# Performance work log

Hardware: AMD Instinct MI355X
Metric: run time of the kernel (lower is better)

## Reference

```python
import jax, jax.numpy as jnp
import numpy as np

N = 100000   # nodes
E = 600000   # edges (before self loops)
D = 128      # dim_latent = H*F
H = 4        # heads
F = 32       # out_feats per head
L = 3        # num GATConv layers (conv_0 + 2)


def setup_inputs() -> dict:
    key = jax.random.key(0)
    ks = jax.random.split(key, 10)
    return {
        "weights": jax.random.normal(ks[0], (N,), jnp.float32),
        "lin_W": jax.random.normal(ks[1], (D, 1), jnp.float32) * 0.1,
        "lin_b": jnp.zeros((D,), jnp.float32),
        "fc_W": jax.random.normal(ks[2], (L, D, D), jnp.float32) * (1.0 / np.sqrt(D)),
        "attn_l": jax.random.normal(ks[3], (L, H, F), jnp.float32) * 0.1,
        "attn_r": jax.random.normal(ks[4], (L, H, F), jnp.float32) * 0.1,
        "conv_b": jnp.zeros((L, D), jnp.float32),
        "pred_W": jax.random.normal(ks[5], (1, D), jnp.float32) * 0.1,
        "pred_b": jnp.zeros((1,), jnp.float32),
        "src": jax.random.randint(ks[6], (E,), 0, N, jnp.int32),
        "dst": jax.random.randint(ks[7], (E,), 0, N, jnp.int32),
    }


def _leaky(x, slope):
    return jnp.where(x >= 0, x, slope * x)


def _gat_conv(x, fc_W, attn_l, attn_r, bias, src, dst):
    # DGL GATConv: bias-free fc, per-head additive attention, edge softmax over dst
    h = (x @ fc_W.T).reshape(N, H, F)                      # [N,H,F]
    el = jnp.sum(h * attn_l[None], axis=-1)                # [N,H]
    er = jnp.sum(h * attn_r[None], axis=-1)                # [N,H]
    e = _leaky(el[src] + er[dst], 0.2)                     # [Etot,H]
    m = jax.ops.segment_max(e, dst, num_segments=N)        # [N,H]
    a = jnp.exp(e - m[dst])                                # [Etot,H]
    s = jax.ops.segment_sum(a, dst, num_segments=N)        # [N,H]
    alpha = a / s[dst]                                     # [Etot,H]
    msg = h[src] * alpha[:, :, None]                       # [Etot,H,F]
    out = jax.ops.segment_sum(msg, dst, num_segments=N)    # [N,H,F]
    out = out + bias.reshape(H, F)[None]
    return out.reshape(N, H * F)


def reference(weights, lin_W, lin_b, fc_W, attn_l, attn_r, conv_b, pred_W, pred_b, src, dst):
    # add self loops (dgl.add_self_loop)
    loop = jnp.arange(N, dtype=src.dtype)
    s_full = jnp.concatenate([src, loop])
    d_full = jnp.concatenate([dst, loop])

    x = weights[:, None] @ lin_W.T + lin_b                 # [N,D]
    for i in range(L):
        if i > 0:
            x = _leaky(x, 0.01)                            # nn.LeakyReLU default
        x = _gat_conv(x, fc_W[i], attn_l[i], attn_r[i], conv_b[i], s_full, d_full)
    logits = x @ pred_W.T + pred_b                         # [N,1]
    return logits
```

## Files before the change

### kernel.cpp

```cpp
#include <hip/hip_runtime.h>
#include <hip/hip_bf16.h>
#include <math.h>


__device__ __forceinline__ float leaky02(float x) {
    return x >= 0.f ? x : 0.2f * x;
}
__device__ __forceinline__ float leaky01(float x) {
    return x >= 0.f ? x : 0.01f * x;
}

__device__ __forceinline__ unsigned short f2bf(float f) {
    unsigned u = __float_as_uint(f);
    unsigned r = u + 0x7FFFu + ((u >> 16) & 1u);
    return (unsigned short)(r >> 16);
}
__device__ __forceinline__ float bf2f(unsigned short s) {
    return __uint_as_float(((unsigned)s) << 16);
}

typedef __attribute__((ext_vector_type(8))) short bf16x8;
typedef __attribute__((ext_vector_type(8))) unsigned short u16x8;
typedef __attribute__((ext_vector_type(4))) float f32x4;

__global__ __launch_bounds__(256) void init_split_kernel(
    int* __restrict__ deg, int N, const float* __restrict__ W,
    short* __restrict__ Wh, short* __restrict__ Wl, int n)
{
    int i = blockIdx.x * 256 + threadIdx.x;
    if (i < N) deg[i] = 1;
    if (i < n) {
        int l    = i >> 14;
        int p    = i & 16383;
        int j    = p & 7;
        int lane = (p >> 3) & 63;
        int c    = (p >> 9) & 7;
        int kk   = p >> 12;
        int mr   = lane & 15;
        int quad = lane >> 4;
        int row  = c * 16 + mr;
        int d    = kk * 32 + quad * 8 + j;
        float f = W[(size_t)l * 16384 + row * 128 + d];
        unsigned short hi = f2bf(f);
        Wh[i] = (short)hi;
        Wl[i] = (short)f2bf(f - bf2f(hi));
    }
}

__global__ __launch_bounds__(1024) void mlr_prep_kernel(
    const float* __restrict__ fc_W, const float* __restrict__ attn_l,
    const float* __restrict__ attn_r, short* __restrict__ Mh,
    short* __restrict__ Ml)
{
    int l = blockIdx.x;
    const float* W  = fc_W + (size_t)(l + 1) * 16384;
    const float* al = attn_l + (l + 1) * 128;
    const float* ar = attn_r + (l + 1) * 128;
    short* mh = Mh + (size_t)l * 16 * 128;
    short* ml = Ml + (size_t)l * 16 * 128;
    int t = threadIdx.x;
    int r = t >> 7;
    int d = t & 127;
    int hh = r & 3;
    const float* av = (r < 4) ? al : ar;
    float s = 0.f;
#pragma unroll
    for (int f = 0; f < 32; ++f)
        s += W[(size_t)(hh * 32 + f) * 128 + d] * av[hh * 32 + f];
    unsigned short hi = f2bf(s);
    mh[r * 128 + d] = (short)hi;
    ml[r * 128 + d] = (short)f2bf(s - bf2f(hi));
    mh[(r + 8) * 128 + d] = 0;
    ml[(r + 8) * 128 + d] = 0;
}

__global__ __launch_bounds__(256) void deg_count_slot_kernel(
    const int* __restrict__ dst, int* __restrict__ deg,
    int* __restrict__ slot, int E)
{
    int i = blockIdx.x * 256 + threadIdx.x;
    if (i < E) slot[i] = atomicAdd(&deg[dst[i]], 1);
}

#define SCAN_TILE 1024

__global__ __launch_bounds__(256) void scanA_kernel(
    const int* __restrict__ deg, int* __restrict__ bsum, int N)
{
    __shared__ int ws[4];
    int b = blockIdx.x, t = threadIdx.x;
    int base = b * SCAN_TILE + t * 4;
    int s = 0;
#pragma unroll
    for (int k = 0; k < 4; ++k) {
        int i = base + k;
        if (i < N) s += deg[i];
    }
#pragma unroll
    for (int m = 32; m >= 1; m >>= 1) s += __shfl_xor(s, m, 64);
    if ((t & 63) == 0) ws[t >> 6] = s;
    __syncthreads();
    if (t == 0) bsum[b] = ws[0] + ws[1] + ws[2] + ws[3];
}

__global__ __launch_bounds__(1024) void scanB_kernel(
    int* __restrict__ bsum, int* __restrict__ bpre, int* __restrict__ rowp,
    int NB, int N)
{
    __shared__ int sh[1024];
    int t = threadIdx.x;
    int v = (t < NB) ? bsum[t] : 0;
    sh[t] = v;
    __syncthreads();
    for (int off = 1; off < 1024; off <<= 1) {
        int u = (t >= off) ? sh[t - off] : 0;
        __syncthreads();
        sh[t] += u;
        __syncthreads();
    }
    if (t < NB) bpre[t] = sh[t] - v;
    if (t == 1023) rowp[N] = sh[1023];
}

__global__ __launch_bounds__(256) void scanC_kernel(
    const int* __restrict__ deg, const int* __restrict__ bpre,
    int* __restrict__ rowp, int* __restrict__ col, int N)
{
    __shared__ int sh[256];
    int b = blockIdx.x, t = threadIdx.x;
    int base = b * SCAN_TILE + t * 4;
    int v[4];
#pragma unroll
    for (int k = 0; k < 4; ++k) {
        int i = base + k;
        v[k] = (i < N) ? deg[i] : 0;
    }
    int tsum = v[0] + v[1] + v[2] + v[3];
    sh[t] = tsum;
    __syncthreads();
    for (int off = 1; off < 256; off <<= 1) {
        int u = (t >= off) ? sh[t - off] : 0;
        __syncthreads();
        sh[t] += u;
        __syncthreads();
    }
    int pre = bpre[b] + sh[t] - tsum;
#pragma unroll
    for (int k = 0; k < 4; ++k) {
        int i = base + k;
        if (i < N) {
            rowp[i] = pre;
            col[pre] = i;
        }
        pre += v[k];
    }
}

__global__ __launch_bounds__(256) void scatter2_kernel(
    const int* __restrict__ src, const int* __restrict__ dst,
    const int* __restrict__ slot, const int* __restrict__ rowp,
    int* __restrict__ col, int E)
{
    int i = blockIdx.x * 256 + threadIdx.x;
    if (i < E) col[rowp[dst[i]] + slot[i]] = src[i];
}

__global__ __launch_bounds__(1024) void rank1_prep_kernel(
    const float* __restrict__ lW, const float* __restrict__ lb,
    const float* __restrict__ W0, const float* __restrict__ al,
    const float* __restrict__ ar, const float* __restrict__ cb2,
    const float* __restrict__ pW, const float* __restrict__ pb,
    float* __restrict__ c1, float* __restrict__ c2, float* __restrict__ prm)
{
    __shared__ float sh1[128], sh2[128], sh3[128], sh4[128], sh5[128];
    int t = threadIdx.x;
    int j = t >> 3, sub = t & 7;
    float s1 = 0.f, s2 = 0.f;
    int d0 = sub * 16;
#pragma unroll
    for (int k = 0; k < 16; ++k) {
        float wv = W0[j * 128 + d0 + k];
        s1 += lW[d0 + k] * wv;
        s2 += lb[d0 + k] * wv;
    }
#pragma unroll
    for (int m = 1; m <= 4; m <<= 1) {
        s1 += __shfl_xor(s1, m, 64);
        s2 += __shfl_xor(s2, m, 64);
    }
    if (sub == 0) {
        c1[j] = s1; c2[j] = s2;
        sh1[j] = s1 * al[j]; sh2[j] = s2 * al[j];
        sh3[j] = s1 * ar[j]; sh4[j] = s2 * ar[j];
        sh5[j] = cb2[j] * pW[j];
    }
    __syncthreads();
    if (t < 4) {
        float p = 0.f, q = 0.f, r = 0.f, s = 0.f;
        for (int f = 0; f < 32; ++f) {
            p += sh1[t * 32 + f]; q += sh2[t * 32 + f];
            r += sh3[t * 32 + f]; s += sh4[t * 32 + f];
        }
        prm[t] = p; prm[4 + t] = q; prm[8 + t] = r; prm[12 + t] = s;
    }
    if (t == 0) {
        float cs = 0.f;
        for (int k = 0; k < 128; ++k) cs += sh5[k];
        prm[16] = cs + pb[0];
    }
}

__global__ __launch_bounds__(256) void agg0_kernel(
    const float* __restrict__ w, const float* __restrict__ c1,
    const float* __restrict__ c2, const float* __restrict__ prm,
    const int* __restrict__ rowp, const int* __restrict__ col,
    const float* __restrict__ bias, unsigned short* __restrict__ xout, int N)
{
    const int lane = threadIdx.x & 63;
    const int q    = lane >> 4;
    const int l16  = lane & 15;
    const int v    = blockIdx.x * 16 + (threadIdx.x >> 6) * 4 + q;
    if (v >= N) return;

    const int r0 = rowp[v], r1 = rowp[v + 1];
    const int head = l16 >> 2;
    const int f0   = l16 * 8;
    const float pl = prm[head],     ql = prm[4 + head];
    const float pr = prm[8 + head], qr = prm[12 + head];

    const float wv  = w[v];
    const float erq = wv * pr + qr;
    const float mref = leaky02(wv * pl + ql + erq);

    float S = 0.f, Sw = 0.f;
    float w_cur = wv;
    for (int j = r0; j < r1; ++j) {
        int jn = (j + 1 < r1) ? (j + 1) : j;
        float w_nxt = w[col[jn]];

        float e = leaky02(w_cur * pl + ql + erq);
        float d = fminf(e - mref, 80.f);
        float p = __expf(d);
        S += p; Sw += p * w_cur;
        w_cur = w_nxt;
    }
    const float t = Sw / S;

    float4 a0 = *reinterpret_cast<const float4*>(&c1[f0]);
    float4 a1 = *reinterpret_cast<const float4*>(&c1[f0 + 4]);
    float4 g0 = *reinterpret_cast<const float4*>(&c2[f0]);
    float4 g1 = *reinterpret_cast<const float4*>(&c2[f0 + 4]);
    float4 b0 = *reinterpret_cast<const float4*>(&bias[f0]);
    float4 b1 = *reinterpret_cast<const float4*>(&bias[f0 + 4]);
    const float aa[8] = {a0.x, a0.y, a0.z, a0.w, a1.x, a1.y, a1.z, a1.w};
    const float gg[8] = {g0.x, g0.y, g0.z, g0.w, g1.x, g1.y, g1.z, g1.w};
    const float bb[8] = {b0.x, b0.y, b0.z, b0.w, b1.x, b1.y, b1.z, b1.w};

    u16x8 o;
#pragma unroll
    for (int k = 0; k < 8; ++k)
        o[k] = f2bf(leaky01(t * aa[k] + gg[k] + bb[k]));
    *reinterpret_cast<u16x8*>(&xout[(size_t)v * 128 + f0]) = o;
}

__global__ __launch_bounds__(256) void gemm_mfma_kernel(
    const unsigned short* __restrict__ xb, const short* __restrict__ Wh,
    const short* __restrict__ Wl, const short* __restrict__ Mh,
    const short* __restrict__ Ml, unsigned short* __restrict__ hb,
    float* __restrict__ el, float* __restrict__ er,
    const float* __restrict__ pW, float* __restrict__ yel,
    int N, int mode)
{
    const int lane = threadIdx.x & 63;
    const int wv   = threadIdx.x >> 6;
    const int m0   = blockIdx.x * 128 + wv * 32;
    const int mr   = lane & 15;
    const int quad = lane >> 4;

    int r0 = m0 + mr;      if (r0 > N - 1) r0 = N - 1;
    int r1 = m0 + 16 + mr; if (r1 > N - 1) r1 = N - 1;
    const unsigned short* xp0 = xb + (size_t)r0 * 128 + quad * 8;
    const unsigned short* xp1 = xb + (size_t)r1 * 128 + quad * 8;

    f32x4 acc0[8], acc1[8], acce0, acce1;
#pragma unroll
    for (int c = 0; c < 8; ++c) {
        acc0[c] = (f32x4){0.f, 0.f, 0.f, 0.f};
        acc1[c] = (f32x4){0.f, 0.f, 0.f, 0.f};
    }
    acce0 = (f32x4){0.f, 0.f, 0.f, 0.f};
    acce1 = (f32x4){0.f, 0.f, 0.f, 0.f};

#pragma unroll
    for (int kk = 0; kk < 4; ++kk) {
        bf16x8 a0 = *reinterpret_cast<const bf16x8*>(xp0 + kk * 32);
        bf16x8 a1 = *reinterpret_cast<const bf16x8*>(xp1 + kk * 32);

        const int kb = kk * 32 + quad * 8;
        bf16x8 bh[8], bl[8];
#pragma unroll
        for (int c = 0; c < 8; ++c) {
            const size_t wo = (size_t)((kk * 8 + c) * 64 + lane) * 8;
            bh[c] = *reinterpret_cast<const bf16x8*>(Wh + wo);
            bl[c] = *reinterpret_cast<const bf16x8*>(Wl + wo);
        }
        bf16x8 eh = *reinterpret_cast<const bf16x8*>(Mh + (size_t)mr * 128 + kb);
        bf16x8 eo = *reinterpret_cast<const bf16x8*>(Ml + (size_t)mr * 128 + kb);
#pragma unroll
        for (int c = 0; c < 8; ++c) {
            acc0[c] = __builtin_amdgcn_mfma_f32_16x16x32_bf16(a0, bh[c], acc0[c], 0, 0, 0);
            acc0[c] = __builtin_amdgcn_mfma_f32_16x16x32_bf16(a0, bl[c], acc0[c], 0, 0, 0);
            acc1[c] = __builtin_amdgcn_mfma_f32_16x16x32_bf16(a1, bh[c], acc1[c], 0, 0, 0);
            acc1[c] = __builtin_amdgcn_mfma_f32_16x16x32_bf16(a1, bl[c], acc1[c], 0, 0, 0);
        }
        acce0 = __builtin_amdgcn_mfma_f32_16x16x32_bf16(a0, eh, acce0, 0, 0, 0);
        acce0 = __builtin_amdgcn_mfma_f32_16x16x32_bf16(a0, eo, acce0, 0, 0, 0);
        acce1 = __builtin_amdgcn_mfma_f32_16x16x32_bf16(a1, eh, acce1, 0, 0, 0);
        acce1 = __builtin_amdgcn_mfma_f32_16x16x32_bf16(a1, eo, acce1, 0, 0, 0);
    }

    if (mode == 0) {
#pragma unroll
        for (int i = 0; i < 4; ++i) {
            int rowA = m0 + quad * 4 + i;
            if (rowA < N) {
                unsigned short* hp = hb + (size_t)rowA * 128 + mr;
#pragma unroll
                for (int c = 0; c < 8; ++c) hp[c * 16] = f2bf(acc0[c][i]);
                if (mr < 4)       el[(size_t)rowA * 4 + mr]       = acce0[i];
                else if (mr < 8)  er[(size_t)rowA * 4 + (mr - 4)] = acce0[i];
            }
            int rowB = m0 + 16 + quad * 4 + i;
            if (rowB < N) {
                unsigned short* hp = hb + (size_t)rowB * 128 + mr;
#pragma unroll
                for (int c = 0; c < 8; ++c) hp[c * 16] = f2bf(acc1[c][i]);
                if (mr < 4)       el[(size_t)rowB * 4 + mr]       = acce1[i];
                else if (mr < 8)  er[(size_t)rowB * 4 + (mr - 4)] = acce1[i];
            }
        }
    } else {
        float pw[8];
#pragma unroll
        for (int c = 0; c < 8; ++c) pw[c] = pW[mr + c * 16];
#pragma unroll
        for (int i = 0; i < 4; ++i) {
            int rowA = m0 + quad * 4 + i;
            {
                float y[4];
#pragma unroll
                for (int h = 0; h < 4; ++h)
                    y[h] = acc0[2 * h][i] * pw[2 * h] + acc0[2 * h + 1][i] * pw[2 * h + 1];
#pragma unroll
                for (int d = 1; d < 16; d <<= 1) {
#pragma unroll
                    for (int h = 0; h < 4; ++h) y[h] += __shfl_xor(y[h], d, 64);
                }
                if (rowA < N) {
                    if (mr < 4) {
                        float2 o; o.x = y[mr]; o.y = acce0[i];
                        *reinterpret_cast<float2*>(&yel[(size_t)rowA * 8 + mr * 2]) = o;
                    } else if (mr < 8) {
                        er[(size_t)rowA * 4 + (mr - 4)] = acce0[i];
                    }
                }
            }
            int rowB = m0 + 16 + quad * 4 + i;
            {
                float y[4];
#pragma unroll
                for (int h = 0; h < 4; ++h)
                    y[h] = acc1[2 * h][i] * pw[2 * h] + acc1[2 * h + 1][i] * pw[2 * h + 1];
#pragma unroll
                for (int d = 1; d < 16; d <<= 1) {
#pragma unroll
                    for (int h = 0; h < 4; ++h) y[h] += __shfl_xor(y[h], d, 64);
                }
                if (rowB < N) {
                    if (mr < 4) {
                        float2 o; o.x = y[mr]; o.y = acce1[i];
                        *reinterpret_cast<float2*>(&yel[(size_t)rowB * 8 + mr * 2]) = o;
                    } else if (mr < 8) {
                        er[(size_t)rowB * 4 + (mr - 4)] = acce1[i];
                    }
                }
            }
        }
    }
}

__global__ __launch_bounds__(256) void agg_mid_kernel(
    const unsigned short* __restrict__ hb, const float* __restrict__ el,
    const float* __restrict__ er, const int* __restrict__ rowp,
    const int* __restrict__ col, const float* __restrict__ bias,
    unsigned short* __restrict__ xout, int N)
{
    const int lane = threadIdx.x & 63;
    const int q    = lane >> 4;
    const int l16  = lane & 15;
    const int v    = blockIdx.x * 16 + (threadIdx.x >> 6) * 4 + q;
    if (v >= N) return;

    const int r0 = rowp[v], r1 = rowp[v + 1];
    const int head = l16 >> 2;
    const int f0   = l16 * 8;
    const float erq = er[(size_t)v * 4 + head];
    const float el_self = el[(size_t)v * 4 + head];
    const float mref = leaky02(el_self + erq);

    float s = 0.f;
    float acc[8];
#pragma unroll
    for (int k = 0; k < 8; ++k) acc[k] = 0.f;

    float elA = el_self;
    u16x8 hvA = *reinterpret_cast<const u16x8*>(&hb[(size_t)v * 128 + f0]);
    int jB = (r0 + 1 < r1) ? r0 + 1 : r1 - 1;
    int uB = col[jB];
    float elB = el[(size_t)uB * 4 + head];
    u16x8 hvB = *reinterpret_cast<const u16x8*>(&hb[(size_t)uB * 128 + f0]);

    for (int j = r0; j < r1; j += 2) {
        int jA2 = (j + 2 < r1) ? j + 2 : r1 - 1;
        int uA2 = col[jA2];
        float elA2 = el[(size_t)uA2 * 4 + head];
        u16x8 hvA2 = *reinterpret_cast<const u16x8*>(&hb[(size_t)uA2 * 128 + f0]);

        {
            float e = leaky02(elA + erq);
            float d = fminf(e - mref, 80.f);
            float p = __expf(d);
            s += p;
#pragma unroll
            for (int k = 0; k < 8; ++k) acc[k] += p * bf2f(hvA[k]);
        }

        if (j + 1 < r1) {
            int jB2 = (j + 3 < r1) ? j + 3 : r1 - 1;
            int uB2 = col[jB2];
            float elB2 = el[(size_t)uB2 * 4 + head];
            u16x8 hvB2 = *reinterpret_cast<const u16x8*>(&hb[(size_t)uB2 * 128 + f0]);

            float e = leaky02(elB + erq);
            float d = fminf(e - mref, 80.f);
            float p = __expf(d);
            s += p;
#pragma unroll
            for (int k = 0; k < 8; ++k) acc[k] += p * bf2f(hvB[k]);

            elB = elB2; hvB = hvB2;
        }
        elA = elA2; hvA = hvA2;
    }
    const float is = 1.f / s;

    float4 b0 = *reinterpret_cast<const float4*>(&bias[f0]);
    float4 b1 = *reinterpret_cast<const float4*>(&bias[f0 + 4]);
    const float bb[8] = {b0.x, b0.y, b0.z, b0.w, b1.x, b1.y, b1.z, b1.w};

    u16x8 o;
#pragma unroll
    for (int k = 0; k < 8; ++k) o[k] = f2bf(leaky01(acc[k] * is + bb[k]));
    *reinterpret_cast<u16x8*>(&xout[(size_t)v * 128 + f0]) = o;
}

__global__ __launch_bounds__(256) void agg2_kernel(
    const float* __restrict__ yel, const float* __restrict__ er,
    const int* __restrict__ rowp, const int* __restrict__ col,
    const float* __restrict__ prm, float* __restrict__ logits, int N)
{
    const int lane = threadIdx.x & 63;
    const int q    = lane >> 4;
    const int l16  = lane & 15;
    const int v    = blockIdx.x * 16 + (threadIdx.x >> 6) * 4 + q;
    if (v >= N) return;

    const int r0 = rowp[v], r1 = rowp[v + 1];
    const int head = l16 >> 2;
    const float erq = er[(size_t)v * 4 + head];

    float2 curA = *reinterpret_cast<const float2*>(&yel[(size_t)v * 8 + head * 2]);
    const float mref = leaky02(curA.y + erq);

    int jB = (r0 + 1 < r1) ? r0 + 1 : r1 - 1;
    int uB = col[jB];
    float2 curB = *reinterpret_cast<const float2*>(&yel[(size_t)uB * 8 + head * 2]);

    float S = 0.f, Acc = 0.f;
    for (int j = r0; j < r1; j += 2) {
        int jA2 = (j + 2 < r1) ? j + 2 : r1 - 1;
        int uA2 = col[jA2];
        float2 nA = *reinterpret_cast<const float2*>(&yel[(size_t)uA2 * 8 + head * 2]);

        {
            float e = leaky02(curA.y + erq);
            float d = fminf(e - mref, 80.f);
            float p = __expf(d);
            S += p; Acc += p * curA.x;
        }

        if (j + 1 < r1) {
            int jB2 = (j + 3 < r1) ? j + 3 : r1 - 1;
            int uB2 = col[jB2];
            float2 nB = *reinterpret_cast<const float2*>(&yel[(size_t)uB2 * 8 + head * 2]);

            float e = leaky02(curB.y + erq);
            float d = fminf(e - mref, 80.f);
            float p = __expf(d);
            S += p; Acc += p * curB.x;

            curB = nB;
        }
        curA = nA;
    }
    float part = Acc / S;
    part += __shfl_xor(part, 4, 64);
    part += __shfl_xor(part, 8, 64);
    if (l16 == 0) logits[v] = part + prm[16];
}

extern "C" void kernel_launch(void* const* d_in, const int* in_sizes, int n_in,
                              void* d_out, int out_size, void* d_ws, size_t ws_size,
                              hipStream_t stream)
{
    const float* weights = (const float*)d_in[0];
    const float* lin_W   = (const float*)d_in[1];
    const float* lin_b   = (const float*)d_in[2];
    const float* fc_W    = (const float*)d_in[3];
    const float* attn_l  = (const float*)d_in[4];
    const float* attn_r  = (const float*)d_in[5];
    const float* conv_b  = (const float*)d_in[6];
    const float* pred_W  = (const float*)d_in[7];
    const float* pred_b  = (const float*)d_in[8];
    const int*   src     = (const int*)d_in[9];
    const int*   dst     = (const int*)d_in[10];

    const int N = in_sizes[0];
    const int E = in_sizes[9];
    const int NB = (N + SCAN_TILE - 1) / SCAN_TILE;

    unsigned short* xb = (unsigned short*)d_ws;
    unsigned short* hb = xb + (size_t)N * 128;
    float* el  = (float*)(hb + (size_t)N * 128);
    float* er  = el + (size_t)N * 4;
    float* yel = er + (size_t)N * 4;
    float* c1  = yel + (size_t)N * 8;
    float* c2  = c1 + 128;
    float* prm = c2 + 128;
    short* Whs = (short*)(prm + 32);
    short* Wls = Whs + 2 * 16384;
    short* Mhs = Wls + 2 * 16384;
    short* Mls = Mhs + 2 * 2048;
    int*   deg  = (int*)(Mls + 2 * 2048);
    int*   rowp = deg + N;
    int*   slot = rowp + (N + 1);
    int*   col  = slot + E;
    int*   bsum = col + (E + N);
    int*   bpre = bsum + NB;

    init_split_kernel<<<(N + 255) / 256, 256, 0, stream>>>(
        deg, N, fc_W + 16384, Whs, Wls, 2 * 16384);
    mlr_prep_kernel<<<2, 1024, 0, stream>>>(fc_W, attn_l, attn_r, Mhs, Mls);
    deg_count_slot_kernel<<<(E + 255) / 256, 256, 0, stream>>>(dst, deg, slot, E);
    scanA_kernel<<<NB, 256, 0, stream>>>(deg, bsum, N);
    scanB_kernel<<<1, 1024, 0, stream>>>(bsum, bpre, rowp, NB, N);
    scanC_kernel<<<NB, 256, 0, stream>>>(deg, bpre, rowp, col, N);
    scatter2_kernel<<<(E + 255) / 256, 256, 0, stream>>>(src, dst, slot, rowp, col, E);

    rank1_prep_kernel<<<1, 1024, 0, stream>>>(
        lin_W, lin_b, fc_W, attn_l, attn_r, conv_b + 2 * 128, pred_W, pred_b,
        c1, c2, prm);

    agg0_kernel<<<(N + 15) / 16, 256, 0, stream>>>(
        weights, c1, c2, prm, rowp, col, conv_b, xb, N);

    gemm_mfma_kernel<<<(N + 127) / 128, 256, 0, stream>>>(
        xb, Whs, Wls, Mhs, Mls, hb, el, er, pred_W, yel, N, 0);
    agg_mid_kernel<<<(N + 15) / 16, 256, 0, stream>>>(
        hb, el, er, rowp, col, conv_b + 128, xb, N);

    gemm_mfma_kernel<<<(N + 127) / 128, 256, 0, stream>>>(
        xb, Whs + 16384, Wls + 16384, Mhs + 2048, Mls + 2048,
        hb, el, er, pred_W, yel, N, 1);
    agg2_kernel<<<(N + 15) / 16, 256, 0, stream>>>(
        yel, er, rowp, col, prm, (float*)d_out, N);
}
```

Baseline: 274.6 us.

## Merge prep kernels into one launch and split edge loops across lanes

Folds the three small setup kernels (degree init plus weight split, attention-matrix prep, rank-1 constant prep) into a single block-dispatched prep kernel, saving two launches. In agg0 and agg2, each head's four redundant lanes now take every fourth edge and combine partial sums with shuffles, instead of all four walking the whole edge list serially. This shortens the dependent gather chain per node. It drops the explicit software prefetch, and the summation order changes slightly.

Result: faster. 251.8 us (-8.3%).

```diff
diff --git a/kernel.cpp b/kernel.cpp
--- a/kernel.cpp
+++ b/kernel.cpp
@@ -23,55 +23,101 @@
 typedef __attribute__((ext_vector_type(8))) unsigned short u16x8;
 typedef __attribute__((ext_vector_type(4))) float f32x4;
 
-__global__ __launch_bounds__(256) void init_split_kernel(
-    int* __restrict__ deg, int N, const float* __restrict__ W,
-    short* __restrict__ Wh, short* __restrict__ Wl, int n)
-{
-    int i = blockIdx.x * 256 + threadIdx.x;
-    if (i < N) deg[i] = 1;
-    if (i < n) {
-        int l    = i >> 14;
-        int p    = i & 16383;
-        int j    = p & 7;
-        int lane = (p >> 3) & 63;
-        int c    = (p >> 9) & 7;
-        int kk   = p >> 12;
-        int mr   = lane & 15;
-        int quad = lane >> 4;
-        int row  = c * 16 + mr;
-        int d    = kk * 32 + quad * 8 + j;
-        float f = W[(size_t)l * 16384 + row * 128 + d];
-        unsigned short hi = f2bf(f);
-        Wh[i] = (short)hi;
-        Wl[i] = (short)f2bf(f - bf2f(hi));
-    }
-}
-
-__global__ __launch_bounds__(1024) void mlr_prep_kernel(
+__global__ __launch_bounds__(1024) void prep_kernel(
+    int* __restrict__ deg, int N,
     const float* __restrict__ fc_W, const float* __restrict__ attn_l,
-    const float* __restrict__ attn_r, short* __restrict__ Mh,
-    short* __restrict__ Ml)
-{
-    int l = blockIdx.x;
-    const float* W  = fc_W + (size_t)(l + 1) * 16384;
-    const float* al = attn_l + (l + 1) * 128;
-    const float* ar = attn_r + (l + 1) * 128;
-    short* mh = Mh + (size_t)l * 16 * 128;
-    short* ml = Ml + (size_t)l * 16 * 128;
-    int t = threadIdx.x;
-    int r = t >> 7;
-    int d = t & 127;
-    int hh = r & 3;
-    const float* av = (r < 4) ? al : ar;
-    float s = 0.f;
-#pragma unroll
-    for (int f = 0; f < 32; ++f)
-        s += W[(size_t)(hh * 32 + f) * 128 + d] * av[hh * 32 + f];
-    unsigned short hi = f2bf(s);
-    mh[r * 128 + d] = (short)hi;
-    ml[r * 128 + d] = (short)f2bf(s - bf2f(hi));
-    mh[(r + 8) * 128 + d] = 0;
-    ml[(r + 8) * 128 + d] = 0;
+    const float* __restrict__ attn_r,
+    short* __restrict__ Wh, short* __restrict__ Wl,
+    short* __restrict__ Mh, short* __restrict__ Ml,
+    const float* __restrict__ lW, const float* __restrict__ lb,
+    const float* __restrict__ cb2, const float* __restrict__ pW,
+    const float* __restrict__ pb,
+    float* __restrict__ c1, float* __restrict__ c2, float* __restrict__ prm)
+{
+    const int nbi = (N + 1023) >> 10;
+    const int b = blockIdx.x;
+    const int t = threadIdx.x;
+
+    if (b < nbi) {
+        int i = b * 1024 + t;
+        if (i < N) deg[i] = 1;
+        if (i < 2 * 16384) {
+            const float* W = fc_W + 16384;
+            int l    = i >> 14;
+            int p    = i & 16383;
+            int j    = p & 7;
+            int lane = (p >> 3) & 63;
+            int c    = (p >> 9) & 7;
+            int kk   = p >> 12;
+            int mr   = lane & 15;
+            int quad = lane >> 4;
+            int row  = c * 16 + mr;
+            int d    = kk * 32 + quad * 8 + j;
+            float f = W[(size_t)l * 16384 + row * 128 + d];
+            unsigned short hi = f2bf(f);
+            Wh[i] = (short)hi;
+            Wl[i] = (short)f2bf(f - bf2f(hi));
+        }
+    } else if (b < nbi + 2) {
+        int l = b - nbi;
+        const float* W  = fc_W + (size_t)(l + 1) * 16384;
+        const float* al = attn_l + (l + 1) * 128;
+        const float* ar = attn_r + (l + 1) * 128;
+        short* mh = Mh + (size_t)l * 16 * 128;
+        short* ml = Ml + (size_t)l * 16 * 128;
+        int r = t >> 7;
+        int d = t & 127;
+        int hh = r & 3;
+        const float* av = (r < 4) ? al : ar;
+        float s = 0.f;
+#pragma unroll
+        for (int f = 0; f < 32; ++f)
+            s += W[(size_t)(hh * 32 + f) * 128 + d] * av[hh * 32 + f];
+        unsigned short hi = f2bf(s);
+        mh[r * 128 + d] = (short)hi;
+        ml[r * 128 + d] = (short)f2bf(s - bf2f(hi));
+        mh[(r + 8) * 128 + d] = 0;
+        ml[(r + 8) * 128 + d] = 0;
+    } else {
+        __shared__ float sh1[128], sh2[128], sh3[128], sh4[128], sh5[128];
+        const float* W0 = fc_W;
+        const float* al = attn_l;
+        const float* ar = attn_r;
+        int j = t >> 3, sub = t & 7;
+        float s1 = 0.f, s2 = 0.f;
+        int d0 = sub * 16;
+#pragma unroll
+        for (int k = 0; k < 16; ++k) {
+            float wv = W0[j * 128 + d0 + k];
+            s1 += lW[d0 + k] * wv;
+            s2 += lb[d0 + k] * wv;
+        }
+#pragma unroll
+        for (int m = 1; m <= 4; m <<= 1) {
+            s1 += __shfl_xor(s1, m, 64);
+            s2 += __shfl_xor(s2, m, 64);
+        }
+        if (sub == 0) {
+            c1[j] = s1; c2[j] = s2;
+            sh1[j] = s1 * al[j]; sh2[j] = s2 * al[j];
+            sh3[j] = s1 * ar[j]; sh4[j] = s2 * ar[j];
+            sh5[j] = cb2[j] * pW[j];
+        }
+        __syncthreads();
+        if (t < 4) {
+            float p = 0.f, q = 0.f, r = 0.f, s = 0.f;
+            for (int f = 0; f < 32; ++f) {
+                p += sh1[t * 32 + f]; q += sh2[t * 32 + f];
+                r += sh3[t * 32 + f]; s += sh4[t * 32 + f];
+            }
+            prm[t] = p; prm[4 + t] = q; prm[8 + t] = r; prm[12 + t] = s;
+        }
+        if (t == 0) {
+            float cs = 0.f;
+            for (int k = 0; k < 128; ++k) cs += sh5[k];
+            prm[16] = cs + pb[0];
+        }
+    }
 }
 
 __global__ __launch_bounds__(256) void deg_count_slot_kernel(
@@ -165,51 +211,6 @@
     if (i < E) col[rowp[dst[i]] + slot[i]] = src[i];
 }
 
-__global__ __launch_bounds__(1024) void rank1_prep_kernel(
-    const float* __restrict__ lW, const float* __restrict__ lb,
-    const float* __restrict__ W0, const float* __restrict__ al,
-    const float* __restrict__ ar, const float* __restrict__ cb2,
-    const float* __restrict__ pW, const float* __restrict__ pb,
-    float* __restrict__ c1, float* __restrict__ c2, float* __restrict__ prm)
-{
-    __shared__ float sh1[128], sh2[128], sh3[128], sh4[128], sh5[128];
-    int t = threadIdx.x;
-    int j = t >> 3, sub = t & 7;
-    float s1 = 0.f, s2 = 0.f;
-    int d0 = sub * 16;
-#pragma unroll
-    for (int k = 0; k < 16; ++k) {
-        float wv = W0[j * 128 + d0 + k];
-        s1 += lW[d0 + k] * wv;
-        s2 += lb[d0 + k] * wv;
-    }
-#pragma unroll
-    for (int m = 1; m <= 4; m <<= 1) {
-        s1 += __shfl_xor(s1, m, 64);
-        s2 += __shfl_xor(s2, m, 64);
-    }
-    if (sub == 0) {
-        c1[j] = s1; c2[j] = s2;
-        sh1[j] = s1 * al[j]; sh2[j] = s2 * al[j];
-        sh3[j] = s1 * ar[j]; sh4[j] = s2 * ar[j];
-        sh5[j] = cb2[j] * pW[j];
-    }
-    __syncthreads();
-    if (t < 4) {
-        float p = 0.f, q = 0.f, r = 0.f, s = 0.f;
-        for (int f = 0; f < 32; ++f) {
-            p += sh1[t * 32 + f]; q += sh2[t * 32 + f];
-            r += sh3[t * 32 + f]; s += sh4[t * 32 + f];
-        }
-        prm[t] = p; prm[4 + t] = q; prm[8 + t] = r; prm[12 + t] = s;
-    }
-    if (t == 0) {
-        float cs = 0.f;
-        for (int k = 0; k < 128; ++k) cs += sh5[k];
-        prm[16] = cs + pb[0];
-    }
-}
-
 __global__ __launch_bounds__(256) void agg0_kernel(
     const float* __restrict__ w, const float* __restrict__ c1,
     const float* __restrict__ c2, const float* __restrict__ prm,
@@ -224,6 +225,7 @@
 
     const int r0 = rowp[v], r1 = rowp[v + 1];
     const int head = l16 >> 2;
+    const int e4   = l16 & 3;
     const int f0   = l16 * 8;
     const float pl = prm[head],     ql = prm[4 + head];
     const float pr = prm[8 + head], qr = prm[12 + head];
@@ -233,17 +235,16 @@
     const float mref = leaky02(wv * pl + ql + erq);
 
     float S = 0.f, Sw = 0.f;
-    float w_cur = wv;
-    for (int j = r0; j < r1; ++j) {
-        int jn = (j + 1 < r1) ? (j + 1) : j;
-        float w_nxt = w[col[jn]];
-
-        float e = leaky02(w_cur * pl + ql + erq);
+    for (int j = r0 + e4; j < r1; j += 4) {
+        int u = col[j];
+        float wu = w[u];
+        float e = leaky02(wu * pl + ql + erq);
         float d = fminf(e - mref, 80.f);
         float p = __expf(d);
-        S += p; Sw += p * w_cur;
-        w_cur = w_nxt;
-    }
+        S += p; Sw += p * wu;
+    }
+    S  += __shfl_xor(S, 1, 64);  S  += __shfl_xor(S, 2, 64);
+    Sw += __shfl_xor(Sw, 1, 64); Sw += __shfl_xor(Sw, 2, 64);
     const float t = Sw / S;
 
     float4 a0 = *reinterpret_cast<const float4*>(&c1[f0]);
@@ -477,43 +478,24 @@
 
     const int r0 = rowp[v], r1 = rowp[v + 1];
     const int head = l16 >> 2;
+    const int e4   = l16 & 3;
     const float erq = er[(size_t)v * 4 + head];
 
-    float2 curA = *reinterpret_cast<const float2*>(&yel[(size_t)v * 8 + head * 2]);
-    const float mref = leaky02(curA.y + erq);
-
-    int jB = (r0 + 1 < r1) ? r0 + 1 : r1 - 1;
-    int uB = col[jB];
-    float2 curB = *reinterpret_cast<const float2*>(&yel[(size_t)uB * 8 + head * 2]);
-
-    float S = 0.f, Acc = 0.f;
-    for (int j = r0; j < r1; j += 2) {
-        int jA2 = (j + 2 < r1) ? j + 2 : r1 - 1;
-        int uA2 = col[jA2];
-        float2 nA = *reinterpret_cast<const float2*>(&yel[(size_t)uA2 * 8 + head * 2]);
-
-        {
-            float e = leaky02(curA.y + erq);
-            float d = fminf(e - mref, 80.f);
-            float p = __expf(d);
-            S += p; Acc += p * curA.x;
-        }
-
-        if (j + 1 < r1) {
-            int jB2 = (j + 3 < r1) ? j + 3 : r1 - 1;
-            int uB2 = col[jB2];
-            float2 nB = *reinterpret_cast<const float2*>(&yel[(size_t)uB2 * 8 + head * 2]);
-
-            float e = leaky02(curB.y + erq);
-            float d = fminf(e - mref, 80.f);
-            float p = __expf(d);
-            S += p; Acc += p * curB.x;
-
-            curB = nB;
-        }
-        curA = nA;
-    }
-    float part = Acc / S;
+    float2 selfy = *reinterpret_cast<const float2*>(&yel[(size_t)v * 8 + head * 2]);
+    const float mref = leaky02(selfy.y + erq);
+
+    float S = 0.f, A = 0.f;
+    for (int j = r0 + e4; j < r1; j += 4) {
+        int u = col[j];
+        float2 c = *reinterpret_cast<const float2*>(&yel[(size_t)u * 8 + head * 2]);
+        float e = leaky02(c.y + erq);
+        float d = fminf(e - mref, 80.f);
+        float p = __expf(d);
+        S += p; A += p * c.x;
+    }
+    S += __shfl_xor(S, 1, 64); S += __shfl_xor(S, 2, 64);
+    A += __shfl_xor(A, 1, 64); A += __shfl_xor(A, 2, 64);
+    float part = A / S;
     part += __shfl_xor(part, 4, 64);
     part += __shfl_xor(part, 8, 64);
     if (l16 == 0) logits[v] = part + prm[16];
@@ -538,6 +520,7 @@
     const int N = in_sizes[0];
     const int E = in_sizes[9];
     const int NB = (N + SCAN_TILE - 1) / SCAN_TILE;
+    const int NBI = (N + 1023) / 1024;
 
     unsigned short* xb = (unsigned short*)d_ws;
     unsigned short* hb = xb + (size_t)N * 128;
@@ -558,19 +541,16 @@
     int*   bsum = col + (E + N);
     int*   bpre = bsum + NB;
 
-    init_split_kernel<<<(N + 255) / 256, 256, 0, stream>>>(
-        deg, N, fc_W + 16384, Whs, Wls, 2 * 16384);
-    mlr_prep_kernel<<<2, 1024, 0, stream>>>(fc_W, attn_l, attn_r, Mhs, Mls);
+    prep_kernel<<<NBI + 3, 1024, 0, stream>>>(
+        deg, N, fc_W, attn_l, attn_r, Whs, Wls, Mhs, Mls,
+        lin_W, lin_b, conv_b + 2 * 128, pred_W, pred_b, c1, c2, prm);
+
     deg_count_slot_kernel<<<(E + 255) / 256, 256, 0, stream>>>(dst, deg, slot, E);
     scanA_kernel<<<NB, 256, 0, stream>>>(deg, bsum, N);
     scanB_kernel<<<1, 1024, 0, stream>>>(bsum, bpre, rowp, NB, N);
     scanC_kernel<<<NB, 256, 0, stream>>>(deg, bpre, rowp, col, N);
     scatter2_kernel<<<(E + 255) / 256, 256, 0, stream>>>(src, dst, slot, rowp, col, E);
 
-    rank1_prep_kernel<<<1, 1024, 0, stream>>>(
-        lin_W, lin_b, fc_W, attn_l, attn_r, conv_b + 2 * 128, pred_W, pred_b,
-        c1, c2, prm);
-
     agg0_kernel<<<(N + 15) / 16, 256, 0, stream>>>(
         weights, c1, c2, prm, rowp, col, conv_b, xb, N);
 
```
